# Kernel tuning notes

Measured on AMD Instinct MI355X. Metric: run time of the kernel, lower is better.

The kernel has to match this reference:

```python
import jax, jax.numpy as jnp
import numpy as np

B, N, F, C = 8, 256, 59, 128
BOX = 20.0
EPS = 1e-5


def _bn(y, g, b, m, v):
    # eval-mode BatchNorm1d over the channel (last) axis
    return (y - m) * jax.lax.rsqrt(v + EPS) * g + b


def setup_inputs() -> dict:
    key = jax.random.key(0)
    ks = jax.random.split(key, 12)
    x = jax.random.normal(ks[0], (B, N, F), jnp.float32)
    pos = jax.random.uniform(ks[1], (B, N, 3), jnp.float32) * BOX
    nrm = jax.random.normal(ks[2], (B, N, 3), jnp.float32)
    normal = nrm / jnp.linalg.norm(nrm, axis=-1, keepdims=True)
    s_in = 1.0 / np.sqrt(F)
    W_lin = jax.random.normal(ks[3], (C, F), jnp.float32) * s_in
    W_src = jax.random.normal(ks[4], (C, F), jnp.float32) * s_in
    W_dst = jax.random.normal(ks[5], (C, F), jnp.float32) * s_in
    pos_w = jax.random.normal(ks[6], (C, 6), jnp.float32) * (1.0 / np.sqrt(6.0))
    pos_b = jax.random.normal(ks[7], (C,), jnp.float32) * 0.02
    attn_w = jax.random.normal(ks[8], (C, C), jnp.float32) * (1.0 / np.sqrt(C))
    attn_b = jax.random.normal(ks[9], (C,), jnp.float32) * 0.02
    pos_bn_g = 1.0 + 0.1 * jax.random.normal(ks[10], (C,), jnp.float32)
    attn_bn_g = 1.0 + 0.1 * jax.random.normal(ks[11], (C,), jnp.float32)
    zeros = jnp.zeros((C,), jnp.float32)
    ones = jnp.ones((C,), jnp.float32)
    return {
        'x': x, 'pos': pos, 'normal': normal,
        'W_lin': W_lin, 'W_src': W_src, 'W_dst': W_dst,
        'pos_w': pos_w, 'pos_b': pos_b,
        'pos_bn_g': pos_bn_g, 'pos_bn_b': zeros, 'pos_bn_m': zeros, 'pos_bn_v': ones,
        'attn_w': attn_w, 'attn_b': attn_b,
        'attn_bn_g': attn_bn_g, 'attn_bn_b': zeros, 'attn_bn_m': zeros, 'attn_bn_v': ones,
        'r': 5,
    }


def reference(x, pos, normal, W_lin, W_src, W_dst, pos_w, pos_b,
              pos_bn_g, pos_bn_b, pos_bn_m, pos_bn_v,
              attn_w, attn_b, attn_bn_g, attn_bn_b, attn_bn_m, attn_bn_v, r):
    r = jnp.float32(r)
    # linear projections (bias-free, as in PyG PointTransformerConv)
    v = jnp.einsum('bnf,cf->bnc', x, W_lin)      # values
    a_src = jnp.einsum('bnf,cf->bnc', x, W_src)  # alpha for source j
    a_dst = jnp.einsum('bnf,cf->bnc', x, W_dst)  # alpha for dest   i
    # relative geometry, axis 1 = receiver i, axis 2 = sender j
    rel_pos = pos[:, :, None, :] - pos[:, None, :, :]          # [B,i,j,3]
    rel_nrm = normal[:, :, None, :] - normal[:, None, :, :]    # [B,i,j,3]
    relf = jnp.concatenate([rel_pos, rel_nrm], axis=-1)        # [B,i,j,6]
    # pos_nn = Linear(6,C) + BN + ReLU (eval)
    delta = jax.nn.relu(_bn(jnp.einsum('bijk,ck->bijc', relf, pos_w) + pos_b,
                            pos_bn_g, pos_bn_b, pos_bn_m, pos_bn_v))
    # attn_nn(alpha_i - alpha_j + delta)
    alpha_arg = a_dst[:, :, None, :] - a_src[:, None, :, :] + delta
    scores = jax.nn.relu(_bn(jnp.einsum('bijc,dc->bijd', alpha_arg, attn_w) + attn_b,
                             attn_bn_g, attn_bn_b, attn_bn_m, attn_bn_v))
    # radius mask within each graph (self-loops included, dist 0 <= r)
    dist2 = jnp.sum(rel_pos * rel_pos, axis=-1)                # [B,i,j]
    mask = (dist2 <= r * r)[..., None]                         # [B,i,j,1]
    attn = jax.nn.softmax(jnp.where(mask, scores, -jnp.inf), axis=2)
    # per-channel vector attention over neighbors j: sum_j attn * (v_j + delta)
    out = jnp.sum(attn * (v[:, None, :, :] + delta), axis=2)   # [B,i,C]
    return out
```

## Files before the change

### kernel.cpp

```cpp
#include <hip/hip_runtime.h>

typedef _Float16 h2 __attribute__((ext_vector_type(2)));
typedef unsigned int uint32;

#define BB 8
#define NN 256
#define FF 59
#define CC 128
#define EPSV 1e-5f
#define MAXJ 96

#define WS_V     0
#define WS_ASRC  (WS_V + BB*NN*CC)
#define WS_ADST  (WS_ASRC + BB*NN*CC)
#define WS_PWT   (WS_ADST + BB*NN*CC)
#define WS_T1    (WS_PWT + 6*CC)
#define WS_T2    (WS_T1 + CC)
#define WS_WTH   (WS_T2 + CC)

#if __has_builtin(__builtin_amdgcn_fdot2)
#define FDOT2(a, b, c) __builtin_amdgcn_fdot2((a), (b), (c), false)
#else
static __device__ __forceinline__ float fdot2_emul(h2 a, h2 b, float c) {
    return c + (float)a.x * (float)b.x + (float)a.y * (float)b.y;
}
#define FDOT2 fdot2_emul
#endif

static __device__ __forceinline__ h2 as_h2(uint32 u) {
    return __builtin_bit_cast(h2, u);
}

__global__ __launch_bounds__(256) void prep_kernel(
    const float* __restrict__ x, const float* __restrict__ W_lin,
    const float* __restrict__ W_src, const float* __restrict__ W_dst,
    const float* __restrict__ pos_w, const float* __restrict__ pos_b,
    const float* __restrict__ pos_g, const float* __restrict__ pos_bb,
    const float* __restrict__ pos_m, const float* __restrict__ pos_v,
    const float* __restrict__ attn_w, const float* __restrict__ attn_b,
    const float* __restrict__ attn_g, const float* __restrict__ attn_bb,
    const float* __restrict__ attn_m, const float* __restrict__ attn_v,
    float* __restrict__ ws)
{
    int blk = blockIdx.x;
    int tid = threadIdx.x;
    if (blk < 768) {
        int type = blk >> 8;
        int g    = blk & 255;
        int b    = g >> 5;
        int n0   = (g & 31) * 8;
        const float* W = (type == 0) ? W_lin : (type == 1) ? W_src : W_dst;
        float* outp = ws + ((type == 0) ? WS_V : (type == 1) ? WS_ASRC : WS_ADST);
        __shared__ float Wl[CC * 60];
        __shared__ float xs[8 * 60];
        for (int idx = tid; idx < CC * 60; idx += 256) {
            int r = idx / 60, f = idx - r * 60;
            Wl[idx] = (f < FF) ? W[r * FF + f] : 0.f;
        }
        const float* xrow = x + (size_t)(b * NN + n0) * FF;
        for (int idx = tid; idx < 8 * 60; idx += 256) {
            int r = idx / 60, f = idx - r * 60;
            xs[idx] = (f < FF) ? xrow[r * FF + f] : 0.f;
        }
        __syncthreads();
        int c = tid & 127, h = tid >> 7;
        float acc[4];
#pragma unroll
        for (int q = 0; q < 4; ++q) acc[q] = 0.f;
#pragma unroll 3
        for (int f4 = 0; f4 < 15; ++f4) {
            float4 wq = *(const float4*)&Wl[c * 60 + f4 * 4];
#pragma unroll
            for (int q = 0; q < 4; ++q) {
                float4 xq = *(const float4*)&xs[(h * 4 + q) * 60 + f4 * 4];
                acc[q] = fmaf(wq.x, xq.x, acc[q]);
                acc[q] = fmaf(wq.y, xq.y, acc[q]);
                acc[q] = fmaf(wq.z, xq.z, acc[q]);
                acc[q] = fmaf(wq.w, xq.w, acc[q]);
            }
        }
#pragma unroll
        for (int q = 0; q < 4; ++q) {
            int n = n0 + h * 4 + q;
            outp[(b * NN + n) * CC + c] = acc[q];
        }
    } else {
        __shared__ float S2s[CC];
        if (tid < CC) {
            int c = tid;
            float S1 = rsqrtf(pos_v[c] + EPSV) * pos_g[c];
            ws[WS_T1 + c] = (pos_b[c] - pos_m[c]) * S1 + pos_bb[c];
#pragma unroll
            for (int k = 0; k < 6; ++k) ws[WS_PWT + k * CC + c] = pos_w[c * 6 + k] * S1;
            float S2 = rsqrtf(attn_v[c] + EPSV) * attn_g[c];
            S2s[c] = S2;
            ws[WS_T2 + c] = (attn_b[c] - attn_m[c]) * S2 + attn_bb[c];
        }
        __syncthreads();
        uint32* wthp = (uint32*)ws + WS_WTH;
        for (int idx = tid; idx < 64 * CC; idx += 256) {
            int p = idx & 63, d = idx >> 6;
            float s = S2s[d];
            float2 w2 = *(const float2*)&attn_w[d * CC + 2 * p];
            h2 hv;
            hv.x = (_Float16)(w2.x * s);
            hv.y = (_Float16)(w2.y * s);
            wthp[p * CC + d] = __builtin_bit_cast(uint32, hv);
        }
    }
}

__global__ __launch_bounds__(256, 4) void main_kernel(
    const float* __restrict__ pos, const float* __restrict__ nrm,
    const int* __restrict__ rptr, const float* __restrict__ ws,
    float* __restrict__ out)
{
    const float* v    = ws + WS_V;
    const float* asrc = ws + WS_ASRC;
    const float* adst = ws + WS_ADST;
    const float* pwt  = ws + WS_PWT;
    const float* T1   = ws + WS_T1;
    const float* T2   = ws + WS_T2;
    const uint32* wth = (const uint32*)ws + WS_WTH;

    int tid  = threadIdx.x;
    int wv   = tid >> 6;
    int lane = tid & 63;
    int gid  = blockIdx.x * 4 + wv;
    int b = gid >> 8, i = gid & 255;
    int cA = lane, cB = lane + 64;

    __shared__ float    relbuf[4][MAXJ * 6];
    __shared__ int      jbuf[4][MAXJ];
    __shared__ _Float16 alpha[4][8 * 136];

    float* relw = relbuf[wv];
    int*   jw   = jbuf[wv];
    _Float16* alw = alpha[wv];

    int rv = rptr[0];
    float r2 = (float)(rv * rv);
    const float* pib = pos + (size_t)(b * NN + i) * 3;
    const float* nib = nrm + (size_t)(b * NN + i) * 3;
    float pix = pib[0], piy = pib[1], piz = pib[2];
    float nix = nib[0], niy = nib[1], niz = nib[2];

    int cnt = 0;
#pragma unroll
    for (int ch = 0; ch < 4; ++ch) {
        int j = ch * 64 + lane;
        const float* pj = pos + (size_t)(b * NN + j) * 3;
        const float* nj = nrm + (size_t)(b * NN + j) * 3;
        float dx = pix - pj[0], dy = piy - pj[1], dz = piz - pj[2];
        float ex = nix - nj[0], ey = niy - nj[1], ez = niz - nj[2];
        float d2 = dx * dx + dy * dy + dz * dz;
        bool valid = (d2 <= r2);
        unsigned long long m = __ballot(valid);
        int rank = __popcll(m & ((1ull << lane) - 1ull));
        int s = cnt + rank;
        if (valid && s < MAXJ) {
            jw[s] = j;
            float2* rp = (float2*)&relw[s * 6];
            rp[0] = make_float2(dx, dy);
            rp[1] = make_float2(dz, ex);
            rp[2] = make_float2(ey, ez);
        }
        cnt += __popcll(m);
    }
    if (cnt > MAXJ) cnt = MAXJ;

    float pwA[6], pwB[6];
#pragma unroll
    for (int k = 0; k < 6; ++k) {
        pwA[k] = pwt[k * CC + cA];
        pwB[k] = pwt[k * CC + cB];
    }
    float T1A = T1[cA], T1B = T1[cB];
    float T2A = T2[cA], T2B = T2[cB];
    int ibase = (b * NN + i) * CC;
    float adA = adst[ibase + cA], adB = adst[ibase + cB];

    float seA = 0.f, seB = 0.f, ovA = 0.f, ovB = 0.f;

    for (int base = 0; base < cnt; base += 8) {
        int ns = cnt - base; if (ns > 8) ns = 8;
        float uA[8], uB[8];
#pragma unroll
        for (int q = 0; q < 8; ++q) {
            float aA = 0.f, aB = 0.f;
            uA[q] = 0.f; uB[q] = 0.f;
            if (q < ns) {
                int j = jw[base + q];
                const float2* rp = (const float2*)&relw[(base + q) * 6];
                float2 r0 = rp[0], r1 = rp[1], r2f = rp[2];
                float dA = T1A, dB = T1B;
                dA = fmaf(pwA[0], r0.x, dA); dB = fmaf(pwB[0], r0.x, dB);
                dA = fmaf(pwA[1], r0.y, dA); dB = fmaf(pwB[1], r0.y, dB);
                dA = fmaf(pwA[2], r1.x, dA); dB = fmaf(pwB[2], r1.x, dB);
                dA = fmaf(pwA[3], r1.y, dA); dB = fmaf(pwB[3], r1.y, dB);
                dA = fmaf(pwA[4], r2f.x, dA); dB = fmaf(pwB[4], r2f.x, dB);
                dA = fmaf(pwA[5], r2f.y, dA); dB = fmaf(pwB[5], r2f.y, dB);
                float deA = fmaxf(dA, 0.f), deB = fmaxf(dB, 0.f);
                int off = (b * NN + j) * CC;
                aA = adA - asrc[off + cA] + deA;
                aB = adB - asrc[off + cB] + deB;
                uA[q] = v[off + cA] + deA;
                uB[q] = v[off + cB] + deB;
            }
            alw[q * 136 + cA] = (_Float16)aA;
            alw[q * 136 + cB] = (_Float16)aB;
        }
        float accA[8], accB[8];
#pragma unroll
        for (int q = 0; q < 8; ++q) { accA[q] = T2A; accB[q] = T2B; }
#pragma unroll 4
        for (int pq = 0; pq < 16; ++pq) {
            uint32 wA0 = wth[(pq * 4 + 0) * CC + cA];
            uint32 wA1 = wth[(pq * 4 + 1) * CC + cA];
            uint32 wA2 = wth[(pq * 4 + 2) * CC + cA];
            uint32 wA3 = wth[(pq * 4 + 3) * CC + cA];
            uint32 wB0 = wth[(pq * 4 + 0) * CC + cB];
            uint32 wB1 = wth[(pq * 4 + 1) * CC + cB];
            uint32 wB2 = wth[(pq * 4 + 2) * CC + cB];
            uint32 wB3 = wth[(pq * 4 + 3) * CC + cB];
#pragma unroll
            for (int q = 0; q < 8; ++q) {
                uint4 av = *(const uint4*)&alw[q * 136 + pq * 8];
                accA[q] = FDOT2(as_h2(av.x), as_h2(wA0), accA[q]);
                accA[q] = FDOT2(as_h2(av.y), as_h2(wA1), accA[q]);
                accA[q] = FDOT2(as_h2(av.z), as_h2(wA2), accA[q]);
                accA[q] = FDOT2(as_h2(av.w), as_h2(wA3), accA[q]);
                accB[q] = FDOT2(as_h2(av.x), as_h2(wB0), accB[q]);
                accB[q] = FDOT2(as_h2(av.y), as_h2(wB1), accB[q]);
                accB[q] = FDOT2(as_h2(av.z), as_h2(wB2), accB[q]);
                accB[q] = FDOT2(as_h2(av.w), as_h2(wB3), accB[q]);
            }
        }
#pragma unroll
        for (int q = 0; q < 8; ++q) {
            if (q < ns) {
                float eA = __expf(fmaxf(accA[q], 0.f));
                float eB = __expf(fmaxf(accB[q], 0.f));
                seA += eA; ovA = fmaf(eA, uA[q], ovA);
                seB += eB; ovB = fmaf(eB, uB[q], ovB);
            }
        }
    }

    out[(size_t)ibase + cA] = ovA / seA;
    out[(size_t)ibase + cB] = ovB / seB;
}

extern "C" void kernel_launch(void* const* d_in, const int* in_sizes, int n_in,
                              void* d_out, int out_size, void* d_ws, size_t ws_size,
                              hipStream_t stream) {
    const float* x      = (const float*)d_in[0];
    const float* pos    = (const float*)d_in[1];
    const float* normal = (const float*)d_in[2];
    const float* W_lin  = (const float*)d_in[3];
    const float* W_src  = (const float*)d_in[4];
    const float* W_dst  = (const float*)d_in[5];
    const float* pos_w  = (const float*)d_in[6];
    const float* pos_b  = (const float*)d_in[7];
    const float* pos_g  = (const float*)d_in[8];
    const float* pos_bb = (const float*)d_in[9];
    const float* pos_m  = (const float*)d_in[10];
    const float* pos_v  = (const float*)d_in[11];
    const float* attn_w = (const float*)d_in[12];
    const float* attn_b = (const float*)d_in[13];
    const float* attn_g = (const float*)d_in[14];
    const float* attn_bb= (const float*)d_in[15];
    const float* attn_m = (const float*)d_in[16];
    const float* attn_v = (const float*)d_in[17];
    const int*   rptr   = (const int*)d_in[18];
    float* ws  = (float*)d_ws;
    float* out = (float*)d_out;

    prep_kernel<<<dim3(769), dim3(256), 0, stream>>>(
        x, W_lin, W_src, W_dst, pos_w, pos_b, pos_g, pos_bb, pos_m, pos_v,
        attn_w, attn_b, attn_g, attn_bb, attn_m, attn_v, ws);
    main_kernel<<<dim3(512), dim3(256), 0, stream>>>(pos, normal, rptr, ws, out);
}
```

Before: 137.1 us.

## Fuse projection prep into main kernel with per-batch spin barrier

Merges the prep and main kernels into one launch. Each block computes the v/a_src/a_dst projections for its own 4 points, bumps a per-batch atomic counter, builds the BN-folded weights and the fp16 attention weights in shared memory, then spins until all 64 blocks of its batch have finished before the neighbor loop. This removes a kernel launch and the global round trip for the small parameter tables. In exchange it depends on all 512 blocks being co-resident, adds about 40KB of shared memory per block and a launch bound of 2 blocks per CU, and has every block repeat the weight-prep work.

```diff
diff --git a/kernel.cpp b/kernel.cpp
--- a/kernel.cpp
+++ b/kernel.cpp
@@ -13,10 +13,7 @@
 #define WS_V     0
 #define WS_ASRC  (WS_V + BB*NN*CC)
 #define WS_ADST  (WS_ASRC + BB*NN*CC)
-#define WS_PWT   (WS_ADST + BB*NN*CC)
-#define WS_T1    (WS_PWT + 6*CC)
-#define WS_T2    (WS_T1 + CC)
-#define WS_WTH   (WS_T2 + CC)
+#define WS_CNT   (WS_ADST + BB*NN*CC)
 
 #if __has_builtin(__builtin_amdgcn_fdot2)
 #define FDOT2(a, b, c) __builtin_amdgcn_fdot2((a), (b), (c), false)
@@ -31,109 +28,102 @@
     return __builtin_bit_cast(h2, u);
 }
 
-__global__ __launch_bounds__(256) void prep_kernel(
-    const float* __restrict__ x, const float* __restrict__ W_lin,
-    const float* __restrict__ W_src, const float* __restrict__ W_dst,
+__global__ __launch_bounds__(256, 2) void fused_kernel(
+    const float* __restrict__ x, const float* __restrict__ pos,
+    const float* __restrict__ nrm,
+    const float* __restrict__ W_lin, const float* __restrict__ W_src,
+    const float* __restrict__ W_dst,
     const float* __restrict__ pos_w, const float* __restrict__ pos_b,
     const float* __restrict__ pos_g, const float* __restrict__ pos_bb,
     const float* __restrict__ pos_m, const float* __restrict__ pos_v,
     const float* __restrict__ attn_w, const float* __restrict__ attn_b,
     const float* __restrict__ attn_g, const float* __restrict__ attn_bb,
     const float* __restrict__ attn_m, const float* __restrict__ attn_v,
-    float* __restrict__ ws)
-{
-    int blk = blockIdx.x;
-    int tid = threadIdx.x;
-    if (blk < 768) {
-        int type = blk >> 8;
-        int g    = blk & 255;
-        int b    = g >> 5;
-        int n0   = (g & 31) * 8;
-        const float* W = (type == 0) ? W_lin : (type == 1) ? W_src : W_dst;
-        float* outp = ws + ((type == 0) ? WS_V : (type == 1) ? WS_ASRC : WS_ADST);
-        __shared__ float Wl[CC * 60];
-        __shared__ float xs[8 * 60];
-        for (int idx = tid; idx < CC * 60; idx += 256) {
-            int r = idx / 60, f = idx - r * 60;
-            Wl[idx] = (f < FF) ? W[r * FF + f] : 0.f;
-        }
-        const float* xrow = x + (size_t)(b * NN + n0) * FF;
-        for (int idx = tid; idx < 8 * 60; idx += 256) {
-            int r = idx / 60, f = idx - r * 60;
-            xs[idx] = (f < FF) ? xrow[r * FF + f] : 0.f;
-        }
-        __syncthreads();
-        int c = tid & 127, h = tid >> 7;
-        float acc[4];
-#pragma unroll
-        for (int q = 0; q < 4; ++q) acc[q] = 0.f;
-#pragma unroll 3
-        for (int f4 = 0; f4 < 15; ++f4) {
-            float4 wq = *(const float4*)&Wl[c * 60 + f4 * 4];
-#pragma unroll
-            for (int q = 0; q < 4; ++q) {
-                float4 xq = *(const float4*)&xs[(h * 4 + q) * 60 + f4 * 4];
-                acc[q] = fmaf(wq.x, xq.x, acc[q]);
-                acc[q] = fmaf(wq.y, xq.y, acc[q]);
-                acc[q] = fmaf(wq.z, xq.z, acc[q]);
-                acc[q] = fmaf(wq.w, xq.w, acc[q]);
-            }
-        }
-#pragma unroll
-        for (int q = 0; q < 4; ++q) {
-            int n = n0 + h * 4 + q;
-            outp[(b * NN + n) * CC + c] = acc[q];
-        }
-    } else {
-        __shared__ float S2s[CC];
-        if (tid < CC) {
-            int c = tid;
-            float S1 = rsqrtf(pos_v[c] + EPSV) * pos_g[c];
-            ws[WS_T1 + c] = (pos_b[c] - pos_m[c]) * S1 + pos_bb[c];
-#pragma unroll
-            for (int k = 0; k < 6; ++k) ws[WS_PWT + k * CC + c] = pos_w[c * 6 + k] * S1;
-            float S2 = rsqrtf(attn_v[c] + EPSV) * attn_g[c];
-            S2s[c] = S2;
-            ws[WS_T2 + c] = (attn_b[c] - attn_m[c]) * S2 + attn_bb[c];
-        }
-        __syncthreads();
-        uint32* wthp = (uint32*)ws + WS_WTH;
-        for (int idx = tid; idx < 64 * CC; idx += 256) {
-            int p = idx & 63, d = idx >> 6;
-            float s = S2s[d];
-            float2 w2 = *(const float2*)&attn_w[d * CC + 2 * p];
-            h2 hv;
-            hv.x = (_Float16)(w2.x * s);
-            hv.y = (_Float16)(w2.y * s);
-            wthp[p * CC + d] = __builtin_bit_cast(uint32, hv);
-        }
-    }
-}
-
-__global__ __launch_bounds__(256, 4) void main_kernel(
-    const float* __restrict__ pos, const float* __restrict__ nrm,
-    const int* __restrict__ rptr, const float* __restrict__ ws,
+    const int* __restrict__ rptr, float* __restrict__ ws,
     float* __restrict__ out)
 {
-    const float* v    = ws + WS_V;
-    const float* asrc = ws + WS_ASRC;
-    const float* adst = ws + WS_ADST;
-    const float* pwt  = ws + WS_PWT;
-    const float* T1   = ws + WS_T1;
-    const float* T2   = ws + WS_T2;
-    const uint32* wth = (const uint32*)ws + WS_WTH;
-
     int tid  = threadIdx.x;
+    int blk  = blockIdx.x;
+    int b    = blk & 7;
+    int i0   = (blk >> 3) * 4;
     int wv   = tid >> 6;
     int lane = tid & 63;
-    int gid  = blockIdx.x * 4 + wv;
-    int b = gid >> 8, i = gid & 255;
+    int c    = tid & 127;
+    int h    = tid >> 7;
     int cA = lane, cB = lane + 64;
 
+    float* vws    = ws + WS_V;
+    float* asrcws = ws + WS_ASRC;
+    float* adstws = ws + WS_ADST;
+    int*   cntp   = (int*)(ws + WS_CNT);
+
+    __shared__ uint32   bigU[64 * CC];
+    __shared__ float    xs[4 * 60];
+    __shared__ float    S2s[CC];
+    __shared__ float    pwl[6 * CC];
+    __shared__ float    T1l[CC], T2l[CC];
     __shared__ float    relbuf[4][MAXJ * 6];
     __shared__ int      jbuf[4][MAXJ];
     __shared__ _Float16 alpha[4][8 * 136];
 
+    {
+        float* Wl = (float*)bigU;
+        for (int idx = tid; idx < 4 * 60; idx += 256) {
+            int r = idx / 60, f = idx - r * 60;
+            xs[idx] = (f < FF) ? x[(size_t)(b * NN + i0 + r) * FF + f] : 0.f;
+        }
+        const float* Ws[3]  = {W_lin, W_src, W_dst};
+        float*       Os[3]  = {vws, asrcws, adstws};
+#pragma unroll 1
+        for (int t = 0; t < 3; ++t) {
+            const float* W = Ws[t];
+            for (int idx = tid; idx < CC * 60; idx += 256) {
+                int r = idx / 60, f = idx - r * 60;
+                Wl[idx] = (f < FF) ? W[r * FF + f] : 0.f;
+            }
+            __syncthreads();
+            float a0 = 0.f, a1 = 0.f;
+#pragma unroll 3
+            for (int f4 = 0; f4 < 15; ++f4) {
+                float4 wq = ((const float4*)&Wl[c * 60])[f4];
+                float4 x0 = ((const float4*)&xs[(2 * h) * 60])[f4];
+                float4 x1 = ((const float4*)&xs[(2 * h + 1) * 60])[f4];
+                a0 = fmaf(wq.x, x0.x, a0); a1 = fmaf(wq.x, x1.x, a1);
+                a0 = fmaf(wq.y, x0.y, a0); a1 = fmaf(wq.y, x1.y, a1);
+                a0 = fmaf(wq.z, x0.z, a0); a1 = fmaf(wq.z, x1.z, a1);
+                a0 = fmaf(wq.w, x0.w, a0); a1 = fmaf(wq.w, x1.w, a1);
+            }
+            Os[t][(b * NN + i0 + 2 * h) * CC + c]     = a0;
+            Os[t][(b * NN + i0 + 2 * h + 1) * CC + c] = a1;
+            __syncthreads();
+        }
+    }
+    __threadfence();
+    __syncthreads();
+    if (tid == 0) atomicAdd(&cntp[b], 1);
+
+    if (tid < CC) {
+        float S1 = rsqrtf(pos_v[tid] + EPSV) * pos_g[tid];
+        T1l[tid] = (pos_b[tid] - pos_m[tid]) * S1 + pos_bb[tid];
+#pragma unroll
+        for (int k = 0; k < 6; ++k) pwl[k * CC + tid] = pos_w[tid * 6 + k] * S1;
+        float S2 = rsqrtf(attn_v[tid] + EPSV) * attn_g[tid];
+        S2s[tid] = S2;
+        T2l[tid] = (attn_b[tid] - attn_m[tid]) * S2 + attn_bb[tid];
+    }
+    __syncthreads();
+    uint32* wth = bigU;
+    for (int idx = tid; idx < 64 * CC; idx += 256) {
+        int p = idx & 63, d = idx >> 6;
+        float s = S2s[d];
+        float2 w2 = *(const float2*)&attn_w[d * CC + 2 * p];
+        h2 hv;
+        hv.x = (_Float16)(w2.x * s);
+        hv.y = (_Float16)(w2.y * s);
+        wth[p * CC + d] = __builtin_bit_cast(uint32, hv);
+    }
+
+    int i = i0 + wv;
     float* relw = relbuf[wv];
     int*   jw   = jbuf[wv];
     _Float16* alw = alpha[wv];
@@ -169,16 +159,26 @@
     }
     if (cnt > MAXJ) cnt = MAXJ;
 
+    if (tid == 0) {
+        int spins = 0;
+        while (atomicAdd(&cntp[b], 0) < 64 && spins < (1 << 26)) {
+            __builtin_amdgcn_s_sleep(4);
+            ++spins;
+        }
+    }
+    __syncthreads();
+    __threadfence();
+
     float pwA[6], pwB[6];
 #pragma unroll
     for (int k = 0; k < 6; ++k) {
-        pwA[k] = pwt[k * CC + cA];
-        pwB[k] = pwt[k * CC + cB];
-    }
-    float T1A = T1[cA], T1B = T1[cB];
-    float T2A = T2[cA], T2B = T2[cB];
+        pwA[k] = pwl[k * CC + cA];
+        pwB[k] = pwl[k * CC + cB];
+    }
+    float T1A = T1l[cA], T1B = T1l[cB];
+    float T2A = T2l[cA], T2B = T2l[cB];
     int ibase = (b * NN + i) * CC;
-    float adA = adst[ibase + cA], adB = adst[ibase + cB];
+    float adA = adstws[ibase + cA], adB = adstws[ibase + cB];
 
     float seA = 0.f, seB = 0.f, ovA = 0.f, ovB = 0.f;
 
@@ -202,10 +202,10 @@
                 dA = fmaf(pwA[5], r2f.y, dA); dB = fmaf(pwB[5], r2f.y, dB);
                 float deA = fmaxf(dA, 0.f), deB = fmaxf(dB, 0.f);
                 int off = (b * NN + j) * CC;
-                aA = adA - asrc[off + cA] + deA;
-                aB = adB - asrc[off + cB] + deB;
-                uA[q] = v[off + cA] + deA;
-                uB[q] = v[off + cB] + deB;
+                aA = adA - asrcws[off + cA] + deA;
+                aB = adB - asrcws[off + cB] + deB;
+                uA[q] = vws[off + cA] + deA;
+                uB[q] = vws[off + cB] + deB;
             }
             alw[q * 136 + cA] = (_Float16)aA;
             alw[q * 136 + cB] = (_Float16)aB;
@@ -276,8 +276,11 @@
     float* ws  = (float*)d_ws;
     float* out = (float*)d_out;
 
-    prep_kernel<<<dim3(769), dim3(256), 0, stream>>>(
-        x, W_lin, W_src, W_dst, pos_w, pos_b, pos_g, pos_bb, pos_m, pos_v,
-        attn_w, attn_b, attn_g, attn_bb, attn_m, attn_v, ws);
-    main_kernel<<<dim3(512), dim3(256), 0, stream>>>(pos, normal, rptr, ws, out);
-}
+    hipMemsetAsync((char*)d_ws + (size_t)WS_CNT * sizeof(float), 0, 64, stream);
+
+    fused_kernel<<<dim3(512), dim3(256), 0, stream>>>(
+        x, pos, normal, W_lin, W_src, W_dst,
+        pos_w, pos_b, pos_g, pos_bb, pos_m, pos_v,
+        attn_w, attn_b, attn_g, attn_bb, attn_m, attn_v,
+        rptr, ws, out);
+}
```

New measurement: 215.1 us. 56.9% more time.
